# Optimization experiments

Measured on AMD Instinct MI355X. Metric: run time of the kernel, lower is better.

The kernel has to match this reference:

```python
import jax, jax.numpy as jnp
import numpy as np

N_NODES = 400      # total nodes across batch
B = 10             # graphs in batch (40 nodes each)
N_CONFIGS = 1000   # fixed by tile dataset
CONFIG_FEAT_DIM = 24
NODE_FEAT_DIM = 85  # continuous cols; node_feat has +1 col for shape-ele-type idx
N_SHAPE_TYPES = 8
SHAPE_EMB = 4
N_OPS = 120
OP_EMB = 32
H = 64             # h_dim
E = 800            # edges
CAT_DIM = NODE_FEAT_DIM + SHAPE_EMB + OP_EMB + CONFIG_FEAT_DIM  # 145


def _lin(k, i, o):
    return jax.random.normal(k, (i, o), jnp.float32) * (1.0 / np.sqrt(i))


def setup_inputs() -> dict:
    key = jax.random.key(0)
    ks = jax.random.split(key, 32)
    node_cont = jax.random.normal(ks[0], (N_NODES, NODE_FEAT_DIM), jnp.float32)
    shape_type = jax.random.randint(ks[1], (N_NODES, 1), 0, N_SHAPE_TYPES).astype(jnp.float32)
    node_feat = jnp.concatenate([node_cont, shape_type], axis=-1)  # [N, 86]
    node_opcode = jax.random.randint(ks[2], (N_NODES,), 0, N_OPS)
    config_feat = jax.random.normal(ks[3], (B * N_CONFIGS, CONFIG_FEAT_DIM), jnp.float32)
    edge_index = jax.random.randint(ks[4], (2, E), 0, N_NODES)
    batch = jnp.arange(N_NODES) // (N_NODES // B)  # 40 nodes per graph
    inp = dict(
        node_feat=node_feat, node_opcode=node_opcode, config_feat=config_feat,
        edge_index=edge_index, batch=batch,
        op_emb=jax.random.normal(ks[5], (N_OPS, OP_EMB), jnp.float32),
        shape_emb=jax.random.normal(ks[6], (N_SHAPE_TYPES, SHAPE_EMB), jnp.float32),
        W1=_lin(ks[7], CAT_DIM, 2 * H), b1=jnp.zeros((2 * H,), jnp.float32),
        W2=_lin(ks[8], 2 * H, 2 * H), b2=jnp.zeros((2 * H,), jnp.float32),
        Wl0=_lin(ks[9], 2 * H, H), Wr0=_lin(ks[10], 2 * H, H), bg0=jnp.zeros((H,), jnp.float32),
        Wl1=_lin(ks[11], H, H), Wr1=_lin(ks[12], H, H), bg1=jnp.zeros((H,), jnp.float32),
        Wl2=_lin(ks[13], H, H), Wr2=_lin(ks[14], H, H), bg2=jnp.zeros((H,), jnp.float32),
        Wp1=_lin(ks[15], H, H // 2), bp1=jnp.zeros((H // 2,), jnp.float32),
        Wp2=_lin(ks[16], H // 2, 1), bp2=jnp.zeros((1,), jnp.float32),
    )
    return inp


def _sage(x, src, dst, Wl, Wr, b, n):
    # PyG SAGEConv: lin_l(x) + lin_r(mean_{j->i} x_j), applied over [N, C, D]
    agg = jax.ops.segment_sum(x[src], dst, num_segments=n)
    deg = jax.ops.segment_sum(jnp.ones((src.shape[0],), x.dtype), dst, num_segments=n)
    mean = agg / jnp.maximum(deg, 1.0)[:, None, None]
    return x @ Wl + mean @ Wr + b


def reference(node_feat, node_opcode, config_feat, edge_index, batch,
              op_emb, shape_emb, W1, b1, W2, b2,
              Wl0, Wr0, bg0, Wl1, Wr1, bg1, Wl2, Wr2, bg2,
              Wp1, bp1, Wp2, bp2):
    n = node_feat.shape[0]
    cfg = config_feat.reshape(-1, N_CONFIGS, CONFIG_FEAT_DIM)  # [B, 1000, 24]
    ste = shape_emb[node_feat[:, -1].astype(jnp.int32)]        # [N, 4]
    op = op_emb[node_opcode]                                   # [N, 32]
    xn = jnp.concatenate([node_feat[:, :-1], ste, op], axis=-1)  # [N, 121]
    xn = jnp.broadcast_to(xn[:, None, :], (n, N_CONFIGS, xn.shape[-1]))
    xc = cfg[batch]  # repeat_interleave(cfg, n_nodes, dim=0) -> per-node config
    x = jnp.concatenate([xn, xc], axis=-1)                     # [N, 1000, 145]
    x = jax.nn.relu(x @ W1 + b1)
    x = jax.nn.relu(x @ W2 + b2)                               # [N, 1000, 128]
    src, dst = edge_index[0], edge_index[1]
    for Wl, Wr, bg in ((Wl0, Wr0, bg0), (Wl1, Wr1, bg1), (Wl2, Wr2, bg2)):
        x = jax.nn.relu(_sage(x, src, dst, Wl, Wr, bg, n))     # [N, 1000, 64]
    xf = x.reshape(n, -1)                                      # [N, 64000]
    cnt = jax.ops.segment_sum(jnp.ones((n,), xf.dtype), batch, num_segments=B)
    xg = jax.ops.segment_max(xf, batch, num_segments=B) \
         + jax.ops.segment_sum(xf, batch, num_segments=B) / jnp.maximum(cnt, 1.0)[:, None]
    xg = xg.reshape(B, N_CONFIGS, -1)                          # [B, 1000, 64]
    xg = xg / jnp.linalg.norm(xg, axis=-1, keepdims=True)
    out = (jax.nn.relu(xg @ Wp1 + bp1) @ Wp2 + bp2)[..., 0]    # [B, 1000]
    return out
```

## Files before the change

### kernel.cpp

```cpp
#include <hip/hip_runtime.h>
#include <hip/hip_bf16.h>

typedef unsigned short u16;
typedef short bf16x8 __attribute__((ext_vector_type(8)));
typedef float f32x4 __attribute__((ext_vector_type(4)));

#define NN 400
#define NB 10
#define NC 1000
#define CFD 24
#define NFD 85
#define NFROW 86
#define SEDIM 4
#define OEDIM 32
#define XND 121
#define EE 800
#define N_SHAPE_GUARD 7

__device__ __forceinline__ float b2f(u16 u) { return __uint_as_float((unsigned)u << 16); }
__device__ __forceinline__ u16 f2b(float v) {
  unsigned x = __float_as_uint(v);
  return (u16)((x + 0x7fff + ((x >> 16) & 1)) >> 16);
}
__device__ __forceinline__ float ldf(const void* p, int idx, int fz) {
  if (fz) return ((const float*)p)[idx];
  return b2f(((const u16*)p)[idx]);
}
__device__ __forceinline__ void stf(void* p, int idx, int fz, float v) {
  if (fz) { ((float*)p)[idx] = v; return; }
  ((u16*)p)[idx] = f2b(v);
}

__device__ __forceinline__ void detect_wave0(const void* W1, int t, int* flagl) {
  if (t < 64) {
    int wild = 0;
    const u16* wv = (const u16*)W1;
    for (int j = t; j < 512; j += 64) {
      float a = fabsf(b2f(wv[j]));
      if (!(a < 1e4f)) wild++;
    }
    #pragma unroll
    for (int off = 32; off; off >>= 1) wild += __shfl_xor(wild, off);
    if (t == 0) *flagl = (wild > 16) ? 1 : 0;
  }
}

__global__ __launch_bounds__(256) void k_prep_all(
    const void* __restrict__ node_feat, const int* __restrict__ opcode,
    const void* __restrict__ cfg, const int* __restrict__ edge_index,
    const void* __restrict__ op_emb, const void* __restrict__ shape_emb,
    const void* __restrict__ W1, const void* __restrict__ b1,
    const void* __restrict__ W2,
    const void* __restrict__ Wl0, const void* __restrict__ Wr0,
    const void* __restrict__ Wl1, const void* __restrict__ Wr1,
    const void* __restrict__ Wl2, const void* __restrict__ Wr2,
    float* __restrict__ A_node, float* __restrict__ C_cfg,
    u16* __restrict__ W2t, u16* __restrict__ Wc0t,
    u16* __restrict__ Wc1t, u16* __restrict__ Wc2t,
    int* __restrict__ offs, int* __restrict__ srcl) {
  __shared__ int flagl;
  int t = threadIdx.x;
  detect_wave0(W1, t, &flagl);
  __syncthreads();
  int fz = flagl;
  int bid = blockIdx.x;

  if (bid < 313) {
    __shared__ float w1l[CFD * 128];
    __shared__ float cfl[32 * CFD];
    int r0 = bid * 32;
    for (int idx = t; idx < CFD * 128; idx += 256)
      w1l[idx] = ldf(W1, (XND + (idx >> 7)) * 128 + (idx & 127), fz);
    for (int idx = t; idx < 32 * CFD; idx += 256) {
      int r = idx / CFD, k = idx - r * CFD;
      if (r0 + r < 10000) cfl[idx] = ldf(cfg, (r0 + r) * CFD + k, fz);
    }
    __syncthreads();
    for (int idx = t; idx < 4096; idx += 256) {
      int row = idx >> 7, col = idx & 127;
      if (r0 + row < 10000) {
        float acc = 0.f;
        #pragma unroll
        for (int k = 0; k < CFD; k++) acc += cfl[row * CFD + k] * w1l[k * 128 + col];
        C_cfg[(size_t)(r0 + row) * 128 + col] = acc;
      }
    }
    return;
  }
  if (bid < 363) {
    __shared__ float w1m[XND * 128];
    __shared__ float xnl[8 * 128];
    int i0 = (bid - 313) * 8;
    for (int idx = t; idx < XND * 128; idx += 256) w1m[idx] = ldf(W1, idx, fz);
    for (int idx = t; idx < 1024; idx += 256) {
      int node = idx >> 7, tt = idx & 127;
      int i = i0 + node;
      float v = 0.f;
      if (tt < NFD) {
        v = ldf(node_feat, i * NFROW + tt, fz);
      } else if (tt < NFD + SEDIM) {
        int st = (int)ldf(node_feat, i * NFROW + NFD, fz);
        st = min(max(st, 0), N_SHAPE_GUARD);
        v = ldf(shape_emb, st * SEDIM + (tt - NFD), fz);
      } else if (tt < XND) {
        int oc = min(max(opcode[i], 0), 119);
        v = ldf(op_emb, oc * OEDIM + (tt - NFD - SEDIM), fz);
      }
      xnl[idx] = v;
    }
    __syncthreads();
    for (int idx = t; idx < 1024; idx += 256) {
      int node = idx >> 7, tt = idx & 127;
      int i = i0 + node;
      float acc = ldf(b1, tt, fz);
      for (int k = 0; k < XND; k++) acc += xnl[node * 128 + k] * w1m[k * 128 + tt];
      A_node[i * 128 + tt] = acc;
    }
    return;
  }
  if (bid < 555) {
    int idx = (bid - 363) * 256 + t;
    if (idx < 16384) {
      int n = idx >> 7, k = idx & 127;
      W2t[idx] = f2b(ldf(W2, k * 128 + n, fz)); return;
    }
    idx -= 16384;
    if (idx < 16384) {
      int n = idx >> 7, k = idx & 127;
      float v = (n < 64) ? ldf(Wl0, k * 64 + n, fz) : ldf(Wr0, k * 64 + n - 64, fz);
      Wc0t[idx] = f2b(v); return;
    }
    idx -= 16384;
    if (idx < 8192) {
      int n = idx >> 6, k = idx & 63;
      float v = (n < 64) ? ldf(Wl1, k * 64 + n, fz) : ldf(Wr1, k * 64 + n - 64, fz);
      Wc1t[idx] = f2b(v); return;
    }
    idx -= 8192;
    if (idx < 8192) {
      int n = idx >> 6, k = idx & 63;
      float v = (n < 64) ? ldf(Wl2, k * 64 + n, fz) : ldf(Wr2, k * 64 + n - 64, fz);
      Wc2t[idx] = f2b(v); return;
    }
    return;
  }
  {
    __shared__ int cnt[NN];
    __shared__ int offl[NN + 1];
    for (int i = t; i < NN; i += 256) cnt[i] = 0;
    __syncthreads();
    for (int e = t; e < EE; e += 256) {
      int d = edge_index[EE + e] & 511; if (d < NN) atomicAdd(&cnt[d], 1);
    }
    __syncthreads();
    if (t == 0) {
      int s = 0;
      for (int i = 0; i < NN; i++) { offl[i] = s; s += cnt[i]; }
      offl[NN] = s;
    }
    __syncthreads();
    for (int i = t; i < NN; i += 256) cnt[i] = offl[i];
    for (int i = t; i < NN + 1; i += 256) offs[i] = offl[i];
    __syncthreads();
    for (int e = t; e < EE; e += 256) {
      int d = edge_index[EE + e] & 511;
      if (d < NN) {
        int p = atomicAdd(&cnt[d], 1);
        srcl[p] = min(max(edge_index[e], 0), NN - 1);
      }
    }
  }
}

__global__ __launch_bounds__(512, 1) void k_fused(
    const float* __restrict__ A_node, const float* __restrict__ C_cfg,
    const int* __restrict__ batch, const int* __restrict__ offs,
    const int* __restrict__ srcl,
    const u16* __restrict__ W2t, const u16* __restrict__ Wc0t,
    const u16* __restrict__ Wc1t, const u16* __restrict__ Wc2t,
    const void* __restrict__ b2, const void* __restrict__ bg0,
    const void* __restrict__ bg1, const void* __restrict__ bg2,
    const void* __restrict__ Wp1, const void* __restrict__ bp1,
    const void* __restrict__ Wp2, const void* __restrict__ bp2,
    const void* __restrict__ W1d, void* __restrict__ out) {
  __shared__ __align__(16) u16 xbuf[400 * 128];
  __shared__ __align__(16) u16 ybuf[400 * 64];
  __shared__ int offsl[401];
  __shared__ int srcll[EE];
  __shared__ int flagl;

  int c = blockIdx.x;
  int t = threadIdx.x;
  int w = t >> 6, l = t & 63;
  int lm = l & 15, quad = l >> 4;

  detect_wave0(W1d, t, &flagl);
  float* cfgl = (float*)ybuf;
  for (int idx = t; idx < 1280; idx += 512)
    cfgl[idx] = C_cfg[((size_t)(idx >> 7) * NC + c) * 128 + (idx & 127)];
  for (int idx = t; idx < 401; idx += 512) offsl[idx] = offs[idx];
  for (int idx = t; idx < EE; idx += 512) srcll[idx] = srcl[idx];
  __syncthreads();
  int fz = flagl;

  {
    bf16x8 wf[8][4];
    #pragma unroll
    for (int mt = 0; mt < 8; mt++)
      #pragma unroll
      for (int kt = 0; kt < 4; kt++)
        wf[mt][kt] = *reinterpret_cast<const bf16x8*>(W2t + (mt*16 + lm)*128 + kt*32 + quad*8);
    float bv[8][4];
    #pragma unroll
    for (int mt = 0; mt < 8; mt++)
      #pragma unroll
      for (int rg = 0; rg < 4; rg++) bv[mt][rg] = ldf(b2, mt*16 + quad*4 + rg, fz);

    for (int tile = w; tile < 25; tile += 8) {
      int i = tile*16 + lm;
      int b = batch[i] % NB;
      const float* an = A_node + i*128;
      const float* cf = cfgl + b*128;
      bf16x8 bfr[4];
      #pragma unroll
      for (int kt = 0; kt < 4; kt++) {
        int ko = kt*32 + quad*8;
        float4 a0 = *(const float4*)(an + ko);
        float4 a1 = *(const float4*)(an + ko + 4);
        float4 c0 = *(const float4*)(cf + ko);
        float4 c1 = *(const float4*)(cf + ko + 4);
        bf16x8 f;
        f[0] = (short)f2b(fmaxf(a0.x + c0.x, 0.f));
        f[1] = (short)f2b(fmaxf(a0.y + c0.y, 0.f));
        f[2] = (short)f2b(fmaxf(a0.z + c0.z, 0.f));
        f[3] = (short)f2b(fmaxf(a0.w + c0.w, 0.f));
        f[4] = (short)f2b(fmaxf(a1.x + c1.x, 0.f));
        f[5] = (short)f2b(fmaxf(a1.y + c1.y, 0.f));
        f[6] = (short)f2b(fmaxf(a1.z + c1.z, 0.f));
        f[7] = (short)f2b(fmaxf(a1.w + c1.w, 0.f));
        bfr[kt] = f;
      }
      f32x4 acc[8] = {};
      #pragma unroll
      for (int kt = 0; kt < 4; kt++)
        #pragma unroll
        for (int mt = 0; mt < 8; mt++)
          acc[mt] = __builtin_amdgcn_mfma_f32_16x16x32_bf16(wf[mt][kt], bfr[kt], acc[mt], 0, 0, 0);
      #pragma unroll
      for (int mt = 0; mt < 8; mt++) {
        ushort4 s;
        s.x = f2b(fmaxf(acc[mt][0] + bv[mt][0], 0.f));
        s.y = f2b(fmaxf(acc[mt][1] + bv[mt][1], 0.f));
        s.z = f2b(fmaxf(acc[mt][2] + bv[mt][2], 0.f));
        s.w = f2b(fmaxf(acc[mt][3] + bv[mt][3], 0.f));
        int ch = mt*2 + (quad >> 1);
        int chs = ch ^ (i & 7);
        *reinterpret_cast<ushort4*>(&xbuf[i*128 + chs*8 + (quad & 1)*4]) = s;
      }
    }
  }
  __syncthreads();

  {
    bf16x8 wl[4][4], wr[4][4];
    #pragma unroll
    for (int mt = 0; mt < 4; mt++)
      #pragma unroll
      for (int kt = 0; kt < 4; kt++) {
        wl[mt][kt] = *reinterpret_cast<const bf16x8*>(Wc0t + (mt*16 + lm)*128 + kt*32 + quad*8);
        wr[mt][kt] = *reinterpret_cast<const bf16x8*>(Wc0t + (64 + mt*16 + lm)*128 + kt*32 + quad*8);
      }
    float bv[4][4];
    #pragma unroll
    for (int mt = 0; mt < 4; mt++)
      #pragma unroll
      for (int rg = 0; rg < 4; rg++) bv[mt][rg] = ldf(bg0, mt*16 + quad*4 + rg, fz);

    for (int tile = w; tile < 25; tile += 8) {
      int i = tile*16 + lm;
      int o0 = offsl[i], o1 = offsl[i + 1];
      float rd = 1.f / fmaxf((float)(o1 - o0), 1.f);
      bf16x8 xf[4], mf[4];
      #pragma unroll
      for (int kt = 0; kt < 4; kt++)
        xf[kt] = *reinterpret_cast<const bf16x8*>(&xbuf[i*128 + ((kt*4 + quad) ^ (i & 7))*8]);
      float s8[4][8] = {};
      int e = o0;
      for (; e + 1 < o1; e += 2) {
        int sn0 = srcll[e], sn1 = srcll[e + 1];
        bf16x8 z0[4], z1[4];
        #pragma unroll
        for (int kt = 0; kt < 4; kt++) {
          z0[kt] = *reinterpret_cast<const bf16x8*>(&xbuf[sn0*128 + ((kt*4 + quad) ^ (sn0 & 7))*8]);
          z1[kt] = *reinterpret_cast<const bf16x8*>(&xbuf[sn1*128 + ((kt*4 + quad) ^ (sn1 & 7))*8]);
        }
        #pragma unroll
        for (int kt = 0; kt < 4; kt++)
          #pragma unroll
          for (int j = 0; j < 8; j++) {
            s8[kt][j] += b2f((u16)z0[kt][j]);
            s8[kt][j] += b2f((u16)z1[kt][j]);
          }
      }
      if (e < o1) {
        int sn0 = srcll[e];
        #pragma unroll
        for (int kt = 0; kt < 4; kt++) {
          bf16x8 zv = *reinterpret_cast<const bf16x8*>(&xbuf[sn0*128 + ((kt*4 + quad) ^ (sn0 & 7))*8]);
          #pragma unroll
          for (int j = 0; j < 8; j++) s8[kt][j] += b2f((u16)zv[j]);
        }
      }
      #pragma unroll
      for (int kt = 0; kt < 4; kt++) {
        bf16x8 f;
        #pragma unroll
        for (int j = 0; j < 8; j++) f[j] = (short)f2b(s8[kt][j] * rd);
        mf[kt] = f;
      }
      f32x4 acc[4] = {};
      #pragma unroll
      for (int kt = 0; kt < 4; kt++)
        #pragma unroll
        for (int mt = 0; mt < 4; mt++) {
          acc[mt] = __builtin_amdgcn_mfma_f32_16x16x32_bf16(wl[mt][kt], xf[kt], acc[mt], 0, 0, 0);
          acc[mt] = __builtin_amdgcn_mfma_f32_16x16x32_bf16(wr[mt][kt], mf[kt], acc[mt], 0, 0, 0);
        }
      #pragma unroll
      for (int mt = 0; mt < 4; mt++) {
        ushort4 s;
        s.x = f2b(fmaxf(acc[mt][0] + bv[mt][0], 0.f));
        s.y = f2b(fmaxf(acc[mt][1] + bv[mt][1], 0.f));
        s.z = f2b(fmaxf(acc[mt][2] + bv[mt][2], 0.f));
        s.w = f2b(fmaxf(acc[mt][3] + bv[mt][3], 0.f));
        int ch = mt*2 + (quad >> 1);
        int chs = ch ^ (i & 7);
        *reinterpret_cast<ushort4*>(&ybuf[i*64 + chs*8 + (quad & 1)*4]) = s;
      }
    }
  }
  __syncthreads();

  u16* src_buf = ybuf;
  u16* dst_buf = xbuf;
  for (int layer = 0; layer < 2; layer++) {
    const u16* Wt = (layer == 0) ? Wc1t : Wc2t;
    const void* bg = (layer == 0) ? bg1 : bg2;
    bf16x8 wl[4][2], wr[4][2];
    #pragma unroll
    for (int mt = 0; mt < 4; mt++)
      #pragma unroll
      for (int kt = 0; kt < 2; kt++) {
        wl[mt][kt] = *reinterpret_cast<const bf16x8*>(Wt + (mt*16 + lm)*64 + kt*32 + quad*8);
        wr[mt][kt] = *reinterpret_cast<const bf16x8*>(Wt + (64 + mt*16 + lm)*64 + kt*32 + quad*8);
      }
    float bv[4][4];
    #pragma unroll
    for (int mt = 0; mt < 4; mt++)
      #pragma unroll
      for (int rg = 0; rg < 4; rg++) bv[mt][rg] = ldf(bg, mt*16 + quad*4 + rg, fz);

    for (int tile = w; tile < 25; tile += 8) {
      int i = tile*16 + lm;
      int o0 = offsl[i], o1 = offsl[i + 1];
      float rd = 1.f / fmaxf((float)(o1 - o0), 1.f);
      bf16x8 xf[2], mf[2];
      #pragma unroll
      for (int kt = 0; kt < 2; kt++)
        xf[kt] = *reinterpret_cast<const bf16x8*>(&src_buf[i*64 + ((kt*4 + quad) ^ (i & 7))*8]);
      float s8[2][8] = {};
      int e = o0;
      for (; e + 1 < o1; e += 2) {
        int sn0 = srcll[e], sn1 = srcll[e + 1];
        bf16x8 z0[2], z1[2];
        #pragma unroll
        for (int kt = 0; kt < 2; kt++) {
          z0[kt] = *reinterpret_cast<const bf16x8*>(&src_buf[sn0*64 + ((kt*4 + quad) ^ (sn0 & 7))*8]);
          z1[kt] = *reinterpret_cast<const bf16x8*>(&src_buf[sn1*64 + ((kt*4 + quad) ^ (sn1 & 7))*8]);
        }
        #pragma unroll
        for (int kt = 0; kt < 2; kt++)
          #pragma unroll
          for (int j = 0; j < 8; j++) {
            s8[kt][j] += b2f((u16)z0[kt][j]);
            s8[kt][j] += b2f((u16)z1[kt][j]);
          }
      }
      if (e < o1) {
        int sn0 = srcll[e];
        #pragma unroll
        for (int kt = 0; kt < 2; kt++) {
          bf16x8 zv = *reinterpret_cast<const bf16x8*>(&src_buf[sn0*64 + ((kt*4 + quad) ^ (sn0 & 7))*8]);
          #pragma unroll
          for (int j = 0; j < 8; j++) s8[kt][j] += b2f((u16)zv[j]);
        }
      }
      #pragma unroll
      for (int kt = 0; kt < 2; kt++) {
        bf16x8 f;
        #pragma unroll
        for (int j = 0; j < 8; j++) f[j] = (short)f2b(s8[kt][j] * rd);
        mf[kt] = f;
      }
      f32x4 acc[4] = {};
      #pragma unroll
      for (int kt = 0; kt < 2; kt++)
        #pragma unroll
        for (int mt = 0; mt < 4; mt++) {
          acc[mt] = __builtin_amdgcn_mfma_f32_16x16x32_bf16(wl[mt][kt], xf[kt], acc[mt], 0, 0, 0);
          acc[mt] = __builtin_amdgcn_mfma_f32_16x16x32_bf16(wr[mt][kt], mf[kt], acc[mt], 0, 0, 0);
        }
      #pragma unroll
      for (int mt = 0; mt < 4; mt++) {
        ushort4 s;
        s.x = f2b(fmaxf(acc[mt][0] + bv[mt][0], 0.f));
        s.y = f2b(fmaxf(acc[mt][1] + bv[mt][1], 0.f));
        s.z = f2b(fmaxf(acc[mt][2] + bv[mt][2], 0.f));
        s.w = f2b(fmaxf(acc[mt][3] + bv[mt][3], 0.f));
        int ch = mt*2 + (quad >> 1);
        int chs = ch ^ (i & 7);
        *reinterpret_cast<ushort4*>(&dst_buf[i*64 + chs*8 + (quad & 1)*4]) = s;
      }
    }
    __syncthreads();
    u16* tmp = src_buf; src_buf = dst_buf; dst_buf = tmp;
  }

  {
    float* scr  = (float*)xbuf;
    float* wp1s = (float*)&xbuf[4096];
    for (int idx = t; idx < 2048; idx += 512) wp1s[idx] = ldf(Wp1, idx, fz);
    __syncthreads();
    for (int b = w; b < NB; b += 8) {
      int h = l;
      float mx = -3.0e38f, sm = 0.f;
      for (int j = 0; j < 40; j++) {
        int row = b*40 + j;
        int chs = (h >> 3) ^ (row & 7);
        float v = b2f(src_buf[row*64 + chs*8 + (h & 7)]);
        mx = fmaxf(mx, v); sm += v;
      }
      float g = mx + sm * (1.f / 40.f);
      float sq = g * g;
      #pragma unroll
      for (int off = 32; off; off >>= 1) sq += __shfl_xor(sq, off);
      float gn = g * rsqrtf(sq);
      scr[w*64 + h] = gn;
      int j32 = l & 31;
      float hj = ldf(bp1, j32, fz);
      for (int k = 0; k < 64; k++) hj += scr[w*64 + k] * wp1s[k*32 + j32];
      hj = fmaxf(hj, 0.f);
      float contrib = hj * ldf(Wp2, j32, fz);
      #pragma unroll
      for (int off = 32; off; off >>= 1) contrib += __shfl_xor(contrib, off);
      if (l == 0) stf(out, b*NC + c, fz, contrib * 0.5f + ldf(bp2, 0, fz));
    }
  }
}

extern "C" void kernel_launch(void* const* d_in, const int* in_sizes, int n_in,
                              void* d_out, int out_size, void* d_ws, size_t ws_size,
                              hipStream_t stream) {
  const void* node_feat   = d_in[0];
  const int*  node_opcode = (const int*)d_in[1];
  const void* config_feat = d_in[2];
  const int*  edge_index  = (const int*)d_in[3];
  const int*  batch       = (const int*)d_in[4];
  const void* op_emb      = d_in[5];
  const void* shape_emb   = d_in[6];
  const void* W1  = d_in[7];
  const void* b1  = d_in[8];
  const void* W2  = d_in[9];
  const void* b2  = d_in[10];
  const void* Wl0 = d_in[11];
  const void* Wr0 = d_in[12];
  const void* bg0 = d_in[13];
  const void* Wl1 = d_in[14];
  const void* Wr1 = d_in[15];
  const void* bg1 = d_in[16];
  const void* Wl2 = d_in[17];
  const void* Wr2 = d_in[18];
  const void* bg2 = d_in[19];
  const void* Wp1 = d_in[20];
  const void* bp1 = d_in[21];
  const void* Wp2 = d_in[22];
  const void* bp2 = d_in[23];

  char* p = (char*)d_ws;
  float* A_node = (float*)p; p += 400*128*4;
  float* C_cfg  = (float*)p; p += 10000*128*4;
  u16*   W2t    = (u16*)p;   p += 128*128*2;
  u16*   Wc0t   = (u16*)p;   p += 128*128*2;
  u16*   Wc1t   = (u16*)p;   p += 128*64*2;
  u16*   Wc2t   = (u16*)p;   p += 128*64*2;
  int*   offs   = (int*)p;   p += 2048;
  int*   srcl   = (int*)p;   p += 4096;

  k_prep_all<<<dim3(556), dim3(256), 0, stream>>>(
      node_feat, node_opcode, config_feat, edge_index, op_emb, shape_emb,
      W1, b1, W2, Wl0, Wr0, Wl1, Wr1, Wl2, Wr2,
      A_node, C_cfg, W2t, Wc0t, Wc1t, Wc2t, offs, srcl);

  k_fused<<<dim3(1000), dim3(512), 0, stream>>>(
      A_node, C_cfg, batch, offs, srcl, W2t, Wc0t, Wc1t, Wc2t,
      b2, bg0, bg1, bg2, Wp1, bp1, Wp2, bp2, W1, d_out);
}
```

Measured before the change: 333.6 us.

## Sort nodes by degree, use packed bf16 converts, register-tile prep GEMMs

```diff
diff --git a/kernel.cpp b/kernel.cpp
--- a/kernel.cpp
+++ b/kernel.cpp
@@ -21,6 +21,11 @@
 __device__ __forceinline__ u16 f2b(float v) {
   unsigned x = __float_as_uint(v);
   return (u16)((x + 0x7fff + ((x >> 16) & 1)) >> 16);
+}
+__device__ __forceinline__ unsigned f2b2(float lo, float hi) {
+  unsigned r;
+  asm("v_cvt_pk_bf16_f32 %0, %1, %2" : "=v"(r) : "v"(lo), "v"(hi));
+  return r;
 }
 __device__ __forceinline__ float ldf(const void* p, int idx, int fz) {
   if (fz) return ((const float*)p)[idx];
@@ -57,7 +62,8 @@
     float* __restrict__ A_node, float* __restrict__ C_cfg,
     u16* __restrict__ W2t, u16* __restrict__ Wc0t,
     u16* __restrict__ Wc1t, u16* __restrict__ Wc2t,
-    int* __restrict__ offs, int* __restrict__ srcl) {
+    int* __restrict__ offs, int* __restrict__ srcl,
+    int* __restrict__ perm) {
   __shared__ int flagl;
   int t = threadIdx.x;
   detect_wave0(W1, t, &flagl);
@@ -76,13 +82,27 @@
       if (r0 + r < 10000) cfl[idx] = ldf(cfg, (r0 + r) * CFD + k, fz);
     }
     __syncthreads();
-    for (int idx = t; idx < 4096; idx += 256) {
-      int row = idx >> 7, col = idx & 127;
-      if (r0 + row < 10000) {
-        float acc = 0.f;
-        #pragma unroll
-        for (int k = 0; k < CFD; k++) acc += cfl[row * CFD + k] * w1l[k * 128 + col];
-        C_cfg[(size_t)(r0 + row) * 128 + col] = acc;
+    int rg = t >> 5;
+    int cg = t & 31;
+    float acc[4][4] = {};
+    for (int k = 0; k < CFD; k++) {
+      float4 bb = *reinterpret_cast<const float4*>(&w1l[k * 128 + cg * 4]);
+      #pragma unroll
+      for (int ri = 0; ri < 4; ri++) {
+        float a = cfl[(rg * 4 + ri) * CFD + k];
+        acc[ri][0] += a * bb.x;
+        acc[ri][1] += a * bb.y;
+        acc[ri][2] += a * bb.z;
+        acc[ri][3] += a * bb.w;
+      }
+    }
+    #pragma unroll
+    for (int ri = 0; ri < 4; ri++) {
+      int row = r0 + rg * 4 + ri;
+      if (row < 10000) {
+        float4 o;
+        o.x = acc[ri][0]; o.y = acc[ri][1]; o.z = acc[ri][2]; o.w = acc[ri][3];
+        *reinterpret_cast<float4*>(&C_cfg[(size_t)row * 128 + cg * 4]) = o;
       }
     }
     return;
@@ -109,13 +129,22 @@
       xnl[idx] = v;
     }
     __syncthreads();
-    for (int idx = t; idx < 1024; idx += 256) {
-      int node = idx >> 7, tt = idx & 127;
-      int i = i0 + node;
-      float acc = ldf(b1, tt, fz);
-      for (int k = 0; k < XND; k++) acc += xnl[node * 128 + k] * w1m[k * 128 + tt];
-      A_node[i * 128 + tt] = acc;
-    }
+    int ng = t >> 6;
+    int c2 = (t & 63) * 2;
+    float a00 = ldf(b1, c2, fz), a01 = ldf(b1, c2 + 1, fz);
+    float a10 = a00, a11 = a01;
+    for (int k = 0; k < XND; k++) {
+      float2 wv = *reinterpret_cast<const float2*>(&w1m[k * 128 + c2]);
+      float x0 = xnl[(ng * 2) * 128 + k];
+      float x1 = xnl[(ng * 2 + 1) * 128 + k];
+      a00 += x0 * wv.x; a01 += x0 * wv.y;
+      a10 += x1 * wv.x; a11 += x1 * wv.y;
+    }
+    int i = i0 + ng * 2;
+    float2 s0; s0.x = a00; s0.y = a01;
+    float2 s1; s1.x = a10; s1.y = a11;
+    *reinterpret_cast<float2*>(&A_node[i * 128 + c2]) = s0;
+    *reinterpret_cast<float2*>(&A_node[(i + 1) * 128 + c2]) = s1;
     return;
   }
   if (bid < 555) {
@@ -147,16 +176,31 @@
   {
     __shared__ int cnt[NN];
     __shared__ int offl[NN + 1];
+    __shared__ int dbin[64];
     for (int i = t; i < NN; i += 256) cnt[i] = 0;
     __syncthreads();
     for (int e = t; e < EE; e += 256) {
       int d = edge_index[EE + e] & 511; if (d < NN) atomicAdd(&cnt[d], 1);
     }
     __syncthreads();
-    if (t == 0) {
-      int s = 0;
-      for (int i = 0; i < NN; i++) { offl[i] = s; s += cnt[i]; }
-      offl[NN] = s;
+    if (t < 64) {
+      int base = t * 7;
+      int lsum = 0;
+      #pragma unroll
+      for (int k = 0; k < 7; k++) { int n = base + k; if (n < NN) lsum += cnt[n]; }
+      int inc = lsum;
+      #pragma unroll
+      for (int off = 1; off < 64; off <<= 1) {
+        int v = __shfl_up(inc, off);
+        if (t >= off) inc += v;
+      }
+      int run = inc - lsum;
+      #pragma unroll
+      for (int k = 0; k < 7; k++) {
+        int n = base + k;
+        if (n < NN) { offl[n] = run; run += cnt[n]; }
+      }
+      if (t == 63) offl[NN] = run;
     }
     __syncthreads();
     for (int i = t; i < NN; i += 256) cnt[i] = offl[i];
@@ -169,13 +213,36 @@
         srcl[p] = min(max(edge_index[e], 0), NN - 1);
       }
     }
+    for (int i = t; i < 64; i += 256) dbin[i] = 0;
+    __syncthreads();
+    for (int i = t; i < NN; i += 256) {
+      int d = min(offl[i + 1] - offl[i], 63);
+      atomicAdd(&dbin[d], 1);
+    }
+    __syncthreads();
+    if (t < 64) {
+      int v = dbin[t];
+      int inc = v;
+      #pragma unroll
+      for (int off = 1; off < 64; off <<= 1) {
+        int s = __shfl_up(inc, off);
+        if (t >= off) inc += s;
+      }
+      dbin[t] = inc - v;
+    }
+    __syncthreads();
+    for (int i = t; i < NN; i += 256) {
+      int d = min(offl[i + 1] - offl[i], 63);
+      int p = atomicAdd(&dbin[d], 1);
+      perm[p] = i;
+    }
   }
 }
 
 __global__ __launch_bounds__(512, 1) void k_fused(
     const float* __restrict__ A_node, const float* __restrict__ C_cfg,
     const int* __restrict__ batch, const int* __restrict__ offs,
-    const int* __restrict__ srcl,
+    const int* __restrict__ srcl, const int* __restrict__ perm,
     const u16* __restrict__ W2t, const u16* __restrict__ Wc0t,
     const u16* __restrict__ Wc1t, const u16* __restrict__ Wc2t,
     const void* __restrict__ b2, const void* __restrict__ bg0,
@@ -185,8 +252,9 @@
     const void* __restrict__ W1d, void* __restrict__ out) {
   __shared__ __align__(16) u16 xbuf[400 * 128];
   __shared__ __align__(16) u16 ybuf[400 * 64];
-  __shared__ int offsl[401];
+  __shared__ int offsl[NN + 1];
   __shared__ int srcll[EE];
+  __shared__ int perml[NN];
   __shared__ int flagl;
 
   int c = blockIdx.x;
@@ -198,8 +266,9 @@
   float* cfgl = (float*)ybuf;
   for (int idx = t; idx < 1280; idx += 512)
     cfgl[idx] = C_cfg[((size_t)(idx >> 7) * NC + c) * 128 + (idx & 127)];
-  for (int idx = t; idx < 401; idx += 512) offsl[idx] = offs[idx];
+  for (int idx = t; idx < NN + 1; idx += 512) offsl[idx] = offs[idx];
   for (int idx = t; idx < EE; idx += 512) srcll[idx] = srcl[idx];
+  for (int idx = t; idx < NN; idx += 512) perml[idx] = perm[idx];
   __syncthreads();
   int fz = flagl;
 
@@ -217,9 +286,9 @@
       for (int rg = 0; rg < 4; rg++) bv[mt][rg] = ldf(b2, mt*16 + quad*4 + rg, fz);
 
     for (int tile = w; tile < 25; tile += 8) {
-      int i = tile*16 + lm;
+      int i = perml[tile*16 + lm];
       int b = batch[i] % NB;
-      const float* an = A_node + i*128;
+      const float* an = A_node + (size_t)i*128;
       const float* cf = cfgl + b*128;
       bf16x8 bfr[4];
       #pragma unroll
@@ -229,16 +298,12 @@
         float4 a1 = *(const float4*)(an + ko + 4);
         float4 c0 = *(const float4*)(cf + ko);
         float4 c1 = *(const float4*)(cf + ko + 4);
-        bf16x8 f;
-        f[0] = (short)f2b(fmaxf(a0.x + c0.x, 0.f));
-        f[1] = (short)f2b(fmaxf(a0.y + c0.y, 0.f));
-        f[2] = (short)f2b(fmaxf(a0.z + c0.z, 0.f));
-        f[3] = (short)f2b(fmaxf(a0.w + c0.w, 0.f));
-        f[4] = (short)f2b(fmaxf(a1.x + c1.x, 0.f));
-        f[5] = (short)f2b(fmaxf(a1.y + c1.y, 0.f));
-        f[6] = (short)f2b(fmaxf(a1.z + c1.z, 0.f));
-        f[7] = (short)f2b(fmaxf(a1.w + c1.w, 0.f));
-        bfr[kt] = f;
+        union { bf16x8 v; unsigned u[4]; } f;
+        f.u[0] = f2b2(fmaxf(a0.x + c0.x, 0.f), fmaxf(a0.y + c0.y, 0.f));
+        f.u[1] = f2b2(fmaxf(a0.z + c0.z, 0.f), fmaxf(a0.w + c0.w, 0.f));
+        f.u[2] = f2b2(fmaxf(a1.x + c1.x, 0.f), fmaxf(a1.y + c1.y, 0.f));
+        f.u[3] = f2b2(fmaxf(a1.z + c1.z, 0.f), fmaxf(a1.w + c1.w, 0.f));
+        bfr[kt] = f.v;
       }
       f32x4 acc[8] = {};
       #pragma unroll
@@ -248,14 +313,12 @@
           acc[mt] = __builtin_amdgcn_mfma_f32_16x16x32_bf16(wf[mt][kt], bfr[kt], acc[mt], 0, 0, 0);
       #pragma unroll
       for (int mt = 0; mt < 8; mt++) {
-        ushort4 s;
-        s.x = f2b(fmaxf(acc[mt][0] + bv[mt][0], 0.f));
-        s.y = f2b(fmaxf(acc[mt][1] + bv[mt][1], 0.f));
-        s.z = f2b(fmaxf(acc[mt][2] + bv[mt][2], 0.f));
-        s.w = f2b(fmaxf(acc[mt][3] + bv[mt][3], 0.f));
+        uint2 s;
+        s.x = f2b2(fmaxf(acc[mt][0] + bv[mt][0], 0.f), fmaxf(acc[mt][1] + bv[mt][1], 0.f));
+        s.y = f2b2(fmaxf(acc[mt][2] + bv[mt][2], 0.f), fmaxf(acc[mt][3] + bv[mt][3], 0.f));
         int ch = mt*2 + (quad >> 1);
         int chs = ch ^ (i & 7);
-        *reinterpret_cast<ushort4*>(&xbuf[i*128 + chs*8 + (quad & 1)*4]) = s;
+        *reinterpret_cast<uint2*>(&xbuf[i*128 + chs*8 + (quad & 1)*4]) = s;
       }
     }
   }
@@ -277,7 +340,7 @@
       for (int rg = 0; rg < 4; rg++) bv[mt][rg] = ldf(bg0, mt*16 + quad*4 + rg, fz);
 
     for (int tile = w; tile < 25; tile += 8) {
-      int i = tile*16 + lm;
+      int i = perml[tile*16 + lm];
       int o0 = offsl[i], o1 = offsl[i + 1];
       float rd = 1.f / fmaxf((float)(o1 - o0), 1.f);
       bf16x8 xf[4], mf[4];
@@ -313,10 +376,12 @@
       }
       #pragma unroll
       for (int kt = 0; kt < 4; kt++) {
-        bf16x8 f;
-        #pragma unroll
-        for (int j = 0; j < 8; j++) f[j] = (short)f2b(s8[kt][j] * rd);
-        mf[kt] = f;
+        union { bf16x8 v; unsigned u[4]; } f;
+        f.u[0] = f2b2(s8[kt][0] * rd, s8[kt][1] * rd);
+        f.u[1] = f2b2(s8[kt][2] * rd, s8[kt][3] * rd);
+        f.u[2] = f2b2(s8[kt][4] * rd, s8[kt][5] * rd);
+        f.u[3] = f2b2(s8[kt][6] * rd, s8[kt][7] * rd);
+        mf[kt] = f.v;
       }
       f32x4 acc[4] = {};
       #pragma unroll
@@ -328,14 +393,12 @@
         }
       #pragma unroll
       for (int mt = 0; mt < 4; mt++) {
-        ushort4 s;
-        s.x = f2b(fmaxf(acc[mt][0] + bv[mt][0], 0.f));
-        s.y = f2b(fmaxf(acc[mt][1] + bv[mt][1], 0.f));
-        s.z = f2b(fmaxf(acc[mt][2] + bv[mt][2], 0.f));
-        s.w = f2b(fmaxf(acc[mt][3] + bv[mt][3], 0.f));
+        uint2 s;
+        s.x = f2b2(fmaxf(acc[mt][0] + bv[mt][0], 0.f), fmaxf(acc[mt][1] + bv[mt][1], 0.f));
+        s.y = f2b2(fmaxf(acc[mt][2] + bv[mt][2], 0.f), fmaxf(acc[mt][3] + bv[mt][3], 0.f));
         int ch = mt*2 + (quad >> 1);
         int chs = ch ^ (i & 7);
-        *reinterpret_cast<ushort4*>(&ybuf[i*64 + chs*8 + (quad & 1)*4]) = s;
+        *reinterpret_cast<uint2*>(&ybuf[i*64 + chs*8 + (quad & 1)*4]) = s;
       }
     }
   }
@@ -361,7 +424,7 @@
       for (int rg = 0; rg < 4; rg++) bv[mt][rg] = ldf(bg, mt*16 + quad*4 + rg, fz);
 
     for (int tile = w; tile < 25; tile += 8) {
-      int i = tile*16 + lm;
+      int i = perml[tile*16 + lm];
       int o0 = offsl[i], o1 = offsl[i + 1];
       float rd = 1.f / fmaxf((float)(o1 - o0), 1.f);
       bf16x8 xf[2], mf[2];
@@ -397,10 +460,12 @@
       }
       #pragma unroll
       for (int kt = 0; kt < 2; kt++) {
-        bf16x8 f;
-        #pragma unroll
-        for (int j = 0; j < 8; j++) f[j] = (short)f2b(s8[kt][j] * rd);
-        mf[kt] = f;
+        union { bf16x8 v; unsigned u[4]; } f;
+        f.u[0] = f2b2(s8[kt][0] * rd, s8[kt][1] * rd);
+        f.u[1] = f2b2(s8[kt][2] * rd, s8[kt][3] * rd);
+        f.u[2] = f2b2(s8[kt][4] * rd, s8[kt][5] * rd);
+        f.u[3] = f2b2(s8[kt][6] * rd, s8[kt][7] * rd);
+        mf[kt] = f.v;
       }
       f32x4 acc[4] = {};
       #pragma unroll
@@ -412,14 +477,12 @@
         }
       #pragma unroll
       for (int mt = 0; mt < 4; mt++) {
-        ushort4 s;
-        s.x = f2b(fmaxf(acc[mt][0] + bv[mt][0], 0.f));
-        s.y = f2b(fmaxf(acc[mt][1] + bv[mt][1], 0.f));
-        s.z = f2b(fmaxf(acc[mt][2] + bv[mt][2], 0.f));
-        s.w = f2b(fmaxf(acc[mt][3] + bv[mt][3], 0.f));
+        uint2 s;
+        s.x = f2b2(fmaxf(acc[mt][0] + bv[mt][0], 0.f), fmaxf(acc[mt][1] + bv[mt][1], 0.f));
+        s.y = f2b2(fmaxf(acc[mt][2] + bv[mt][2], 0.f), fmaxf(acc[mt][3] + bv[mt][3], 0.f));
         int ch = mt*2 + (quad >> 1);
         int chs = ch ^ (i & 7);
-        *reinterpret_cast<ushort4*>(&dst_buf[i*64 + chs*8 + (quad & 1)*4]) = s;
+        *reinterpret_cast<uint2*>(&dst_buf[i*64 + chs*8 + (quad & 1)*4]) = s;
       }
     }
     __syncthreads();
@@ -495,13 +558,14 @@
   u16*   Wc2t   = (u16*)p;   p += 128*64*2;
   int*   offs   = (int*)p;   p += 2048;
   int*   srcl   = (int*)p;   p += 4096;
+  int*   perm   = (int*)p;   p += 2048;
 
   k_prep_all<<<dim3(556), dim3(256), 0, stream>>>(
       node_feat, node_opcode, config_feat, edge_index, op_emb, shape_emb,
       W1, b1, W2, Wl0, Wr0, Wl1, Wr1, Wl2, Wr2,
-      A_node, C_cfg, W2t, Wc0t, Wc1t, Wc2t, offs, srcl);
+      A_node, C_cfg, W2t, Wc0t, Wc1t, Wc2t, offs, srcl, perm);
 
   k_fused<<<dim3(1000), dim3(512), 0, stream>>>(
-      A_node, C_cfg, batch, offs, srcl, W2t, Wc0t, Wc1t, Wc2t,
+      A_node, C_cfg, batch, offs, srcl, perm, W2t, Wc0t, Wc1t, Wc2t,
       b2, bg0, bg1, bg2, Wp1, bp1, Wp2, bp2, W1, d_out);
 }
```

Result: faster. 306.3 us (median of 3 runs) (-8.2%).
